# Performance work log

Measured on AMD Instinct MI355X. Metric: run time of the kernel, lower is better.

## Reference

```python
import jax, jax.numpy as jnp
import numpy as np

P, B, L = 32, 64, 128
E, HB, HP = 64, 128, 128   # byte emb dim, byte GRU hidden, packet GRU hidden
PE = 2 * HB                # packet embedding dim = 256
LH = 128                   # attention linear hidden
NC = 10                    # num classes


def _gru_dir(x, w_ih, w_hh, b_ih, b_hh, reverse=False):
    # x: [T, N, E_in] -> outputs [T, N, H]; PyTorch GRU gate math, h0 = 0.
    H = w_hh.shape[1]
    xg = jnp.einsum('tne,ge->tng', x, w_ih) + b_ih  # precompute input gates [T,N,3H]
    if reverse:
        xg = xg[::-1]

    def step(h, xgt):
        hg = h @ w_hh.T + b_hh
        xr, xz, xn = jnp.split(xgt, 3, axis=-1)
        hr, hz, hn = jnp.split(hg, 3, axis=-1)
        r = jax.nn.sigmoid(xr + hr)
        z = jax.nn.sigmoid(xz + hz)
        n = jnp.tanh(xn + r * hn)
        h = (1.0 - z) * n + z * h
        return h, h

    h0 = jnp.zeros((x.shape[1], H), x.dtype)
    _, ys = jax.lax.scan(step, h0, xg)
    if reverse:
        ys = ys[::-1]
    return ys


def _bigru(x, wif, whf, bif, bhf, wib, whb, bib, bhb):
    f = _gru_dir(x, wif, whf, bif, bhf, reverse=False)
    b = _gru_dir(x, wib, whb, bib, bhb, reverse=True)
    return jnp.concatenate([f, b], axis=-1)


def setup_inputs() -> dict:
    key = jax.random.key(0)
    ks = jax.random.split(key, 32)
    rn = lambda k, shp: (jax.random.normal(k, shp, dtype=jnp.float32) * 0.05)
    inp = {}
    inp['flow'] = jax.random.randint(ks[0], (P, B, L), 0, 256, dtype=jnp.int64)
    inp['emb'] = rn(ks[1], (256, E))
    # byte biGRU (forward / backward dirs)
    inp['byte_wih_f'] = rn(ks[2], (3 * HB, E)); inp['byte_whh_f'] = rn(ks[3], (3 * HB, HB))
    inp['byte_bih_f'] = rn(ks[4], (3 * HB,));   inp['byte_bhh_f'] = rn(ks[5], (3 * HB,))
    inp['byte_wih_b'] = rn(ks[6], (3 * HB, E)); inp['byte_whh_b'] = rn(ks[7], (3 * HB, HB))
    inp['byte_bih_b'] = rn(ks[8], (3 * HB,));   inp['byte_bhh_b'] = rn(ks[9], (3 * HB,))
    # packet biGRU
    inp['pkt_wih_f'] = rn(ks[10], (3 * HP, PE)); inp['pkt_whh_f'] = rn(ks[11], (3 * HP, HP))
    inp['pkt_bih_f'] = rn(ks[12], (3 * HP,));    inp['pkt_bhh_f'] = rn(ks[13], (3 * HP,))
    inp['pkt_wih_b'] = rn(ks[14], (3 * HP, PE)); inp['pkt_whh_b'] = rn(ks[15], (3 * HP, HP))
    inp['pkt_bih_b'] = rn(ks[16], (3 * HP,));    inp['pkt_bhh_b'] = rn(ks[17], (3 * HP,))
    # byte attention (Linear(2HB->LH), Linear(LH->1))
    inp['ba_w1'] = rn(ks[18], (LH, 2 * HB)); inp['ba_b1'] = rn(ks[19], (LH,))
    inp['ba_w2'] = rn(ks[20], (1, LH));      inp['ba_b2'] = rn(ks[21], (1,))
    # packet attention (Linear(2HP->LH), Linear(LH->1))
    inp['pa_w1'] = rn(ks[22], (LH, 2 * HP)); inp['pa_b1'] = rn(ks[23], (LH,))
    inp['pa_w2'] = rn(ks[24], (1, LH));      inp['pa_b2'] = rn(ks[25], (1,))
    # final classifier
    inp['wf'] = rn(ks[26], (NC, 2 * HP)); inp['bf'] = rn(ks[27], (NC,))
    return inp


def reference(flow, emb,
              byte_wih_f, byte_whh_f, byte_bih_f, byte_bhh_f,
              byte_wih_b, byte_whh_b, byte_bih_b, byte_bhh_b,
              pkt_wih_f, pkt_whh_f, pkt_bih_f, pkt_bhh_f,
              pkt_wih_b, pkt_whh_b, pkt_bih_b, pkt_bhh_b,
              ba_w1, ba_b1, ba_w2, ba_b2,
              pa_w1, pa_b1, pa_w2, pa_b2,
              wf, bf):
    p, b, l = flow.shape
    x = emb[flow]                                   # [P,B,L,E]
    # batch the per-packet byte GRU across packets: [L, P*B, E]
    xb = x.transpose(2, 0, 1, 3).reshape(l, p * b, E)
    out = _bigru(xb, byte_wih_f, byte_whh_f, byte_bih_f, byte_bhh_f,
                 byte_wih_b, byte_whh_b, byte_bih_b, byte_bhh_b)  # [L, P*B, 2HB]
    out = out.reshape(l, p, b, 2 * HB)
    # Attention: tanh(lin1) -> lin2 -> softmax over dim=1 of the [L,B,1] view,
    # i.e. over the batch axis (faithful to the original code).
    h = jnp.tanh(jnp.einsum('lpbd,hd->lpbh', out, ba_w1) + ba_b1)
    score = jnp.einsum('lpbh,oh->lpbo', h, ba_w2) + ba_b2          # [L,P,B,1]
    attn = jax.nn.softmax(score, axis=2)
    packet_emb = (out * attn).sum(axis=0)                          # [P,B,2HB]
    # packet biGRU over packet sequence
    out2 = _bigru(packet_emb, pkt_wih_f, pkt_whh_f, pkt_bih_f, pkt_bhh_f,
                  pkt_wih_b, pkt_whh_b, pkt_bih_b, pkt_bhh_b)      # [P,B,2HP]
    h2 = jnp.tanh(jnp.einsum('pbd,hd->pbh', out2, pa_w1) + pa_b1)
    score2 = jnp.einsum('pbh,oh->pbo', h2, pa_w2) + pa_b2          # [P,B,1]
    attn2 = jax.nn.softmax(score2, axis=1)
    flow_emb = (out2 * attn2).sum(axis=1)                          # [P,2HP] (faithful sum over dim=1)
    return flow_emb @ wf.T + bf                                    # [P,NC]
```

## Files before the change

kernel.cpp:

```cpp
#include <hip/hip_runtime.h>
#include <hip/hip_bf16.h>
#include <hip/hip_fp16.h>
#include <cstdint>
#include <cstddef>


#define DINLINE __device__ __forceinline__

typedef _Float16 f16;
typedef f16 f16x8 __attribute__((ext_vector_type(8)));
typedef float f32x4 __attribute__((ext_vector_type(4)));

static DINLINE float fast_sigmoid(float x) {
    const float e = __builtin_amdgcn_exp2f(-1.44269504089f * x);
    return __builtin_amdgcn_rcpf(1.0f + e);
}
static DINLINE float fast_tanh(float x) {
    const float e = __builtin_amdgcn_exp2f(2.88539008178f * x);
    return 1.0f - 2.0f * __builtin_amdgcn_rcpf(1.0f + e);
}

static DINLINE void lds_barrier() {
    asm volatile("s_waitcnt lgkmcnt(0)\n\ts_barrier" ::: "memory");
}

__global__ void k_tables(const float* __restrict__ emb,
                         const float* __restrict__ wihF, const float* __restrict__ bihF,
                         const float* __restrict__ bhhF,
                         const float* __restrict__ wihB, const float* __restrict__ bihB,
                         const float* __restrict__ bhhB,
                         __half* __restrict__ tab4F, __half* __restrict__ tab4B) {
    const int v = blockIdx.x & 255;
    const int dir = blockIdx.x >> 8;
    const float* wih = dir ? wihB : wihF;
    const float* bih = dir ? bihB : bihF;
    const float* bhh = dir ? bhhB : bhhF;
    __half* tab4 = dir ? tab4B : tab4F;
    __shared__ float er[64];
    __shared__ float sh[384];
    if (threadIdx.x < 64) er[threadIdx.x] = emb[v * 64 + threadIdx.x];
    __syncthreads();
    const int g = threadIdx.x;
    float acc = bih[g] + (g < 256 ? bhh[g] : 0.0f);
    #pragma unroll
    for (int e = 0; e < 64; ++e) acc = fmaf(wih[g * 64 + e], er[e], acc);
    sh[g] = acc;
    __syncthreads();
    if (g < 128) {
        f16 pk[4];
        pk[0] = (f16)sh[g];
        pk[1] = (f16)sh[g + 128];
        pk[2] = (f16)sh[g + 256];
        pk[3] = (f16)0.f;
        *reinterpret_cast<uint2*>(&tab4[(v * 128 + g) * 4]) =
            *reinterpret_cast<const uint2*>(pk);
    }
}

struct TransArgs {
    const float* src[2];
    float* dst[2];
    int R[2];
    int C[2];
};
__global__ void k_transpose(TransArgs a) {
    const int m = blockIdx.y;
    const float* __restrict__ s = a.src[m];
    float* __restrict__ d = a.dst[m];
    const int R = a.R[m], C = a.C[m];
    const int total = R * C;
    for (int idx = blockIdx.x * blockDim.x + threadIdx.x; idx < total;
         idx += gridDim.x * blockDim.x) {
        const int r = idx / C, c = idx - r * C;
        d[c * R + r] = s[idx];
    }
}

__global__ __launch_bounds__(512, 1) void k_byte_gru(
    const int* __restrict__ flow,
    const __half* __restrict__ tab4F, const __half* __restrict__ tab4B,
    const float* __restrict__ whhF, const float* __restrict__ whhB,
    const float* __restrict__ bhhF, const float* __restrict__ bhhB,
    __half* __restrict__ hF, __half* __restrict__ hB) {
    const int dir = blockIdx.x & 1;
    const int chunk = blockIdx.x >> 1;
    const int row0 = chunk * 16;
    const int tid = threadIdx.x;
    const int wid = tid >> 6;
    const int lane = tid & 63;
    const int c = lane & 15;
    const int q = lane >> 4;
    const int j = wid * 16 + c;

    const uint2* __restrict__ t4 =
        reinterpret_cast<const uint2*>(dir ? tab4B : tab4F);
    const float* __restrict__ whh = dir ? whhB : whhF;
    const float* __restrict__ bhh = dir ? bhhB : bhhF;
    __half* __restrict__ hout = dir ? hB : hF;

    __shared__ f16 hbuf[2][16 * 128];
    __shared__ int flow_lds[16][128];

    for (int i = tid; i < 16 * 128; i += 512)
        flow_lds[i >> 7][i & 127] = flow[row0 * 128 + i] & 255;
    for (int i = tid; i < 16 * 128; i += 512) hbuf[0][i] = (f16)0.f;

    f16x8 Bf[3][4];
    #pragma unroll
    for (int g = 0; g < 3; ++g) {
        #pragma unroll
        for (int ks = 0; ks < 4; ++ks) {
            const float* src = whh + (size_t)(g * 128 + j) * 128 + ks * 32 + q * 8;
            f16x8 b;
            #pragma unroll
            for (int e = 0; e < 8; ++e) b[e] = (f16)src[e];
            Bf[g][ks] = b;
        }
    }
    const float bh2 = bhh[j + 256];
    float hold[4];
    #pragma unroll
    for (int rr = 0; rr < 4; ++rr) hold[rr] = 0.f;
    __syncthreads();

    uint2 xg[4];
    {
        const int tt0 = dir ? 127 : 0;
        #pragma unroll
        for (int rr = 0; rr < 4; ++rr)
            xg[rr] = t4[flow_lds[q * 4 + rr][tt0] * 128 + j];
    }

    #pragma unroll 2
    for (int t = 0; t < 128; ++t) {
        const int curb = t & 1, nxtb = curb ^ 1;
        const int tt = dir ? (127 - t) : t;

        f16x8 Af[4];
        #pragma unroll
        for (int ks = 0; ks < 4; ++ks) {
            const int kb = ks * 32 + q * 8;
            const int idx = c * 128 + (kb ^ ((c & 7) << 3));
            Af[ks] = *reinterpret_cast<const f16x8*>(&hbuf[curb][idx]);
        }

        uint2 xgn[4];
        if (t < 127) {
            const int ttn = dir ? (126 - t) : (t + 1);
            #pragma unroll
            for (int rr = 0; rr < 4; ++rr)
                xgn[rr] = t4[flow_lds[q * 4 + rr][ttn] * 128 + j];
        }

        f32x4 a0 = {0.f, 0.f, 0.f, 0.f};
        f32x4 a1 = {0.f, 0.f, 0.f, 0.f};
        f32x4 a2 = {0.f, 0.f, 0.f, 0.f};
        #pragma unroll
        for (int ks = 0; ks < 4; ++ks) {
            a0 = __builtin_amdgcn_mfma_f32_16x16x32_f16(Af[ks], Bf[0][ks], a0, 0, 0, 0);
            a1 = __builtin_amdgcn_mfma_f32_16x16x32_f16(Af[ks], Bf[1][ks], a1, 0, 0, 0);
            a2 = __builtin_amdgcn_mfma_f32_16x16x32_f16(Af[ks], Bf[2][ks], a2, 0, 0, 0);
        }

        #pragma unroll
        for (int rr = 0; rr < 4; ++rr) {
            const f16* xp = reinterpret_cast<const f16*>(&xg[rr]);
            const float rg = fast_sigmoid((float)xp[0] + a0[rr]);
            const float zg = fast_sigmoid((float)xp[1] + a1[rr]);
            const float ng = fast_tanh((float)xp[2] + rg * (a2[rr] + bh2));
            const float hn = fmaf(zg, hold[rr] - ng, ng);
            hold[rr] = hn;
            const int row = q * 4 + rr;
            hbuf[nxtb][row * 128 + (j ^ ((row & 7) << 3))] = (f16)hn;
            hout[((size_t)tt * 2048 + row0 + row) * 128 + j] = (__half)hn;
        }
        lds_barrier();
        #pragma unroll
        for (int rr = 0; rr < 4; ++rr) xg[rr] = xgn[rr];
    }
}

__global__ __launch_bounds__(256, 1) void k_scores_attn(
    const __half* __restrict__ hF, const __half* __restrict__ hB,
    const float* __restrict__ w1,
    const float* __restrict__ b1, const float* __restrict__ w2,
    const float* __restrict__ b2, float* __restrict__ attn) {
    __shared__ f16 w1lds[128 * 256];
    __shared__ float sc[128];
    const int tid = threadIdx.x;
    for (int i = tid; i < 128 * 256; i += 256) {
        const int col = i >> 8, k = i & 255;
        w1lds[col * 256 + (k ^ ((col & 7) << 3))] = (f16)w1[i];
    }
    const int lane = tid & 63, w = tid >> 6;
    const int c = lane & 15, q = lane >> 4;

    float b1v[8], w2v[8];
    #pragma unroll
    for (int ct = 0; ct < 8; ++ct) {
        b1v[ct] = b1[ct * 16 + c];
        w2v[ct] = w2[ct * 16 + c];
    }
    const float b2v = b2[0];
    __syncthreads();

    for (int it = 0; it < 4; ++it) {
        const int pos0 = blockIdx.x * 512 + it * 128;

        f16x8 Af[2][8];
        #pragma unroll
        for (int pt = 0; pt < 2; ++pt) {
            const size_t pos = (size_t)pos0 + (w * 2 + pt) * 16 + c;
            const f16* hFp = (const f16*)(hF + pos * 128);
            const f16* hBp = (const f16*)(hB + pos * 128);
            #pragma unroll
            for (int ks = 0; ks < 4; ++ks)
                Af[pt][ks] = *reinterpret_cast<const f16x8*>(hFp + ks * 32 + q * 8);
            #pragma unroll
            for (int ks = 0; ks < 4; ++ks)
                Af[pt][4 + ks] = *reinterpret_cast<const f16x8*>(hBp + ks * 32 + q * 8);
        }

        float s[2][4] = {{0.f, 0.f, 0.f, 0.f}, {0.f, 0.f, 0.f, 0.f}};
        #pragma unroll
        for (int ct = 0; ct < 8; ++ct) {
            const int jj = ct * 16 + c;
            f16x8 Bfr[8];
            #pragma unroll
            for (int ks = 0; ks < 8; ++ks) {
                const int k = ks * 32 + q * 8;
                Bfr[ks] = *reinterpret_cast<const f16x8*>(
                    &w1lds[jj * 256 + (k ^ ((jj & 7) << 3))]);
            }
            #pragma unroll
            for (int pt = 0; pt < 2; ++pt) {
                f32x4 acc = {0.f, 0.f, 0.f, 0.f};
                #pragma unroll
                for (int ks = 0; ks < 8; ++ks)
                    acc = __builtin_amdgcn_mfma_f32_16x16x32_f16(Af[pt][ks],
                                                                 Bfr[ks], acc,
                                                                 0, 0, 0);
                #pragma unroll
                for (int rr = 0; rr < 4; ++rr)
                    s[pt][rr] += w2v[ct] * fast_tanh(acc[rr] + b1v[ct]);
            }
        }
        #pragma unroll
        for (int pt = 0; pt < 2; ++pt) {
            #pragma unroll
            for (int rr = 0; rr < 4; ++rr) {
                float v = s[pt][rr];
                v += __shfl_xor(v, 1);
                v += __shfl_xor(v, 2);
                v += __shfl_xor(v, 4);
                v += __shfl_xor(v, 8);
                if (c == 0) sc[(w * 2 + pt) * 16 + q * 4 + rr] = v + b2v;
            }
        }
        __syncthreads();
        if (tid < 128) {
            const float sv = sc[tid];
            float m = sv;
            for (int off = 32; off; off >>= 1) m = fmaxf(m, __shfl_xor(m, off));
            const float e = __expf(sv - m);
            float sum = e;
            for (int off = 32; off; off >>= 1) sum += __shfl_xor(sum, off);
            attn[pos0 + tid] = e / sum;
        }
        __syncthreads();
    }
}

__global__ __launch_bounds__(256) void k_packet_emb(
    const __half* __restrict__ hF, const __half* __restrict__ hB,
    const float* __restrict__ attn, float* __restrict__ pe) {
    const int tid = threadIdx.x;
    const int g = tid >> 6;
    const int lane = tid & 63;
    const int n = blockIdx.x * 4 + g;
    const bool isF = lane < 32;
    const int chunk = lane & 31;
    const __half* __restrict__ hsrc = (isF ? hF : hB) + (size_t)n * 128 + chunk * 4;
    float acc0 = 0.f, acc1 = 0.f, acc2 = 0.f, acc3 = 0.f;
    #pragma unroll 4
    for (int l = 0; l < 128; ++l) {
        const float wv = attn[l * 2048 + n];
        const uint2 u = *reinterpret_cast<const uint2*>(hsrc + (size_t)l * 2048 * 128);
        const f16* hv = reinterpret_cast<const f16*>(&u);
        acc0 = fmaf(wv, (float)hv[0], acc0);
        acc1 = fmaf(wv, (float)hv[1], acc1);
        acc2 = fmaf(wv, (float)hv[2], acc2);
        acc3 = fmaf(wv, (float)hv[3], acc3);
    }
    float4 o = {acc0, acc1, acc2, acc3};
    *reinterpret_cast<float4*>(&pe[n * 256 + (isF ? 0 : 128) + chunk * 4]) = o;
}

__global__ __launch_bounds__(384) void k_pkt_xg(
    const float* __restrict__ pe, const float* __restrict__ wihTF,
    const float* __restrict__ bihF, const float* __restrict__ bhhF,
    const float* __restrict__ wihTB, const float* __restrict__ bihB,
    const float* __restrict__ bhhB, float* __restrict__ xgF,
    float* __restrict__ xgB) {
    const int dir = blockIdx.y;
    const float* __restrict__ wihT = dir ? wihTB : wihTF;
    const float* __restrict__ bih = dir ? bihB : bihF;
    const float* __restrict__ bhh = dir ? bhhB : bhhF;
    float* __restrict__ xg = dir ? xgB : xgF;
    const int rbase = blockIdx.x * 8;
    __shared__ float xrow[8][256];
    for (int i = threadIdx.x; i < 8 * 256; i += 384)
        xrow[i >> 8][i & 255] = pe[rbase * 256 + i];
    __syncthreads();
    const int g = threadIdx.x;
    float acc[8];
    const float bias = bih[g] + (g < 256 ? bhh[g] : 0.0f);
    #pragma unroll
    for (int r = 0; r < 8; ++r) acc[r] = bias;
    for (int d = 0; d < 256; ++d) {
        const float w = wihT[d * 384 + g];
        #pragma unroll
        for (int r = 0; r < 8; ++r) acc[r] = fmaf(w, xrow[r][d], acc[r]);
    }
    #pragma unroll
    for (int r = 0; r < 8; ++r) xg[(rbase + r) * 384 + g] = acc[r];
}

__global__ __launch_bounds__(512, 1) void k_pkt_gru(
    const float* __restrict__ xgF, const float* __restrict__ xgB,
    const float* __restrict__ whhF, const float* __restrict__ whhB,
    const float* __restrict__ bhhF, const float* __restrict__ bhhB,
    float* __restrict__ h2F, float* __restrict__ h2B) {
    const int dir = blockIdx.x & 1;
    const int chunk = blockIdx.x >> 1;
    const int row0 = chunk * 16;
    const int tid = threadIdx.x;
    const int wid = tid >> 6;
    const int lane = tid & 63;
    const int c = lane & 15;
    const int q = lane >> 4;
    const int j = wid * 16 + c;

    const float* __restrict__ xg = dir ? xgB : xgF;
    const float* __restrict__ whh = dir ? whhB : whhF;
    const float* __restrict__ bhh = dir ? bhhB : bhhF;
    float* __restrict__ hout = dir ? h2B : h2F;

    __shared__ f16 hbuf[2][16 * 128];

    for (int i = tid; i < 16 * 128; i += 512) hbuf[0][i] = (f16)0.f;

    f16x8 Bf[3][4];
    #pragma unroll
    for (int g = 0; g < 3; ++g) {
        #pragma unroll
        for (int ks = 0; ks < 4; ++ks) {
            const float* src = whh + (size_t)(g * 128 + j) * 128 + ks * 32 + q * 8;
            f16x8 b;
            #pragma unroll
            for (int e = 0; e < 8; ++e) b[e] = (f16)src[e];
            Bf[g][ks] = b;
        }
    }
    const float bh2 = bhh[j + 256];
    float hold[4];
    #pragma unroll
    for (int rr = 0; rr < 4; ++rr) hold[rr] = 0.f;
    __syncthreads();

    for (int t = 0; t < 32; ++t) {
        const int curb = t & 1, nxtb = curb ^ 1;
        const int tt = dir ? (31 - t) : t;

        float xr[4], xz[4], xn[4];
        #pragma unroll
        for (int rr = 0; rr < 4; ++rr) {
            const float* xp = xg + ((size_t)tt * 64 + row0 + q * 4 + rr) * 384 + j;
            xr[rr] = xp[0];
            xz[rr] = xp[128];
            xn[rr] = xp[256];
        }

        f16x8 Af[4];
        #pragma unroll
        for (int ks = 0; ks < 4; ++ks) {
            const int kb = ks * 32 + q * 8;
            const int idx = c * 128 + (kb ^ ((c & 7) << 3));
            Af[ks] = *reinterpret_cast<const f16x8*>(&hbuf[curb][idx]);
        }

        f32x4 a0 = {0.f, 0.f, 0.f, 0.f};
        f32x4 a1 = {0.f, 0.f, 0.f, 0.f};
        f32x4 a2 = {0.f, 0.f, 0.f, 0.f};
        #pragma unroll
        for (int ks = 0; ks < 4; ++ks) {
            a0 = __builtin_amdgcn_mfma_f32_16x16x32_f16(Af[ks], Bf[0][ks], a0, 0, 0, 0);
            a1 = __builtin_amdgcn_mfma_f32_16x16x32_f16(Af[ks], Bf[1][ks], a1, 0, 0, 0);
            a2 = __builtin_amdgcn_mfma_f32_16x16x32_f16(Af[ks], Bf[2][ks], a2, 0, 0, 0);
        }

        #pragma unroll
        for (int rr = 0; rr < 4; ++rr) {
            const float rg = fast_sigmoid(xr[rr] + a0[rr]);
            const float zg = fast_sigmoid(xz[rr] + a1[rr]);
            const float ng = fast_tanh(xn[rr] + rg * (a2[rr] + bh2));
            const float hn = fmaf(zg, hold[rr] - ng, ng);
            hold[rr] = hn;
            const int row = q * 4 + rr;
            hbuf[nxtb][row * 128 + (j ^ ((row & 7) << 3))] = (f16)hn;
            hout[((size_t)tt * 64 + row0 + row) * 128 + j] = hn;
        }
        lds_barrier();
    }
}

__global__ __launch_bounds__(128) void k_scores2(
    const float* __restrict__ h2F, const float* __restrict__ h2B,
    const float* __restrict__ paw1,
    const float* __restrict__ pab1, const float* __restrict__ paw2,
    const float* __restrict__ pab2, float* __restrict__ scores2) {
    const int n = blockIdx.x;
    const int tid = threadIdx.x;
    __shared__ float x[256];
    __shared__ float red[2];
    x[tid] = h2F[n * 128 + tid];
    x[tid + 128] = h2B[n * 128 + tid];
    __syncthreads();
    float acc = pab1[tid];
    const float* wr = paw1 + tid * 256;
    #pragma unroll 8
    for (int d = 0; d < 256; ++d) acc = fmaf(wr[d], x[d], acc);
    float s = paw2[tid] * fast_tanh(acc);
    s += __shfl_xor(s, 1);
    s += __shfl_xor(s, 2);
    s += __shfl_xor(s, 4);
    s += __shfl_xor(s, 8);
    s += __shfl_xor(s, 16);
    s += __shfl_xor(s, 32);
    if ((tid & 63) == 0) red[tid >> 6] = s;
    __syncthreads();
    if (tid == 0) scores2[n] = red[0] + red[1] + pab2[0];
}

__global__ __launch_bounds__(256) void k_final3(
    const float* __restrict__ h2F, const float* __restrict__ h2B,
    const float* __restrict__ scores2, const float* __restrict__ wf,
    const float* __restrict__ bfv, float* __restrict__ outp) {
    const int p = blockIdx.x;
    const int tid = threadIdx.x;
    __shared__ float sc[64];
    __shared__ float femb[256];
    __shared__ float red[64];

    if (tid < 64) {
        const float s = scores2[p * 64 + tid];
        float m = s;
        for (int off = 32; off; off >>= 1) m = fmaxf(m, __shfl_xor(m, off));
        const float e = __expf(s - m);
        float sum = e;
        for (int off = 32; off; off >>= 1) sum += __shfl_xor(sum, off);
        sc[tid] = e / sum;
    }
    __syncthreads();

    {
        const float* __restrict__ hsrc = (tid < 128) ? h2F : h2B;
        const int d = tid & 127;
        float acc = 0.f;
        for (int b = 0; b < 64; ++b)
            acc = fmaf(sc[b], hsrc[(p * 64 + b) * 128 + d], acc);
        femb[tid] = acc;
    }
    __syncthreads();

    const float fv = femb[tid];
    #pragma unroll
    for (int c = 0; c < 10; ++c) {
        float s = fv * wf[c * 256 + tid];
        s += __shfl_xor(s, 1);
        s += __shfl_xor(s, 2);
        s += __shfl_xor(s, 4);
        s += __shfl_xor(s, 8);
        s += __shfl_xor(s, 16);
        s += __shfl_xor(s, 32);
        if ((tid & 63) == 0) red[(c << 2) | (tid >> 6)] = s;
        __syncthreads();
        if (tid == 0)
            outp[p * 10 + c] = bfv[c] + red[c << 2] + red[(c << 2) | 1] +
                               red[(c << 2) | 2] + red[(c << 2) | 3];
        __syncthreads();
    }
}

extern "C" void kernel_launch(void* const* d_in, const int* in_sizes, int n_in,
                              void* d_out, int out_size, void* d_ws,
                              size_t ws_size, hipStream_t stream) {
    const int* flow = (const int*)d_in[0];
    const float* emb = (const float*)d_in[1];
    const float* byte_wih_f = (const float*)d_in[2];
    const float* byte_whh_f = (const float*)d_in[3];
    const float* byte_bih_f = (const float*)d_in[4];
    const float* byte_bhh_f = (const float*)d_in[5];
    const float* byte_wih_b = (const float*)d_in[6];
    const float* byte_whh_b = (const float*)d_in[7];
    const float* byte_bih_b = (const float*)d_in[8];
    const float* byte_bhh_b = (const float*)d_in[9];
    const float* pkt_wih_f = (const float*)d_in[10];
    const float* pkt_whh_f = (const float*)d_in[11];
    const float* pkt_bih_f = (const float*)d_in[12];
    const float* pkt_bhh_f = (const float*)d_in[13];
    const float* pkt_wih_b = (const float*)d_in[14];
    const float* pkt_whh_b = (const float*)d_in[15];
    const float* pkt_bih_b = (const float*)d_in[16];
    const float* pkt_bhh_b = (const float*)d_in[17];
    const float* ba_w1 = (const float*)d_in[18];
    const float* ba_b1 = (const float*)d_in[19];
    const float* ba_w2 = (const float*)d_in[20];
    const float* ba_b2 = (const float*)d_in[21];
    const float* pa_w1 = (const float*)d_in[22];
    const float* pa_b1 = (const float*)d_in[23];
    const float* pa_w2 = (const float*)d_in[24];
    const float* pa_b2 = (const float*)d_in[25];
    const float* wf = (const float*)d_in[26];
    const float* bf = (const float*)d_in[27];

    char* base = (char*)d_ws;
    size_t off = 0;
    auto allocf = [&](size_t nf) -> float* {
        float* p = (float*)(base + off);
        off += nf * sizeof(float);
        return p;
    };
    auto alloch = [&](size_t nh) -> __half* {
        off = (off + 255) & ~(size_t)255;
        __half* p = (__half*)(base + off);
        off += nh * sizeof(__half);
        return p;
    };
    float* wihTpF = allocf(256 * 384);
    float* wihTpB = allocf(256 * 384);
    float* attn = allocf(262144);
    float* pe = allocf(2048 * 256);
    float* xgF = allocf(32 * 64 * 384);
    float* xgB = allocf(32 * 64 * 384);
    float* h2F = allocf(32 * 64 * 128);
    float* h2B = allocf(32 * 64 * 128);
    float* scores2 = allocf(2048);
    __half* tab4F = alloch(256 * 128 * 4);
    __half* tab4B = alloch(256 * 128 * 4);
    __half* hF = alloch((size_t)128 * 2048 * 128);
    __half* hB = alloch((size_t)128 * 2048 * 128);
    if (off > ws_size) return;
    (void)in_sizes; (void)n_in; (void)out_size;

    k_tables<<<512, 384, 0, stream>>>(emb, byte_wih_f, byte_bih_f, byte_bhh_f,
                                      byte_wih_b, byte_bih_b, byte_bhh_b,
                                      tab4F, tab4B);

    TransArgs ta;
    ta.src[0] = pkt_wih_f; ta.dst[0] = wihTpF; ta.R[0] = 384; ta.C[0] = 256;
    ta.src[1] = pkt_wih_b; ta.dst[1] = wihTpB; ta.R[1] = 384; ta.C[1] = 256;
    k_transpose<<<dim3(96, 2), 256, 0, stream>>>(ta);

    k_byte_gru<<<256, 512, 0, stream>>>(flow, tab4F, tab4B, byte_whh_f,
                                        byte_whh_b, byte_bhh_f, byte_bhh_b, hF,
                                        hB);

    k_scores_attn<<<512, 256, 0, stream>>>(hF, hB, ba_w1, ba_b1, ba_w2, ba_b2,
                                           attn);
    k_packet_emb<<<512, 256, 0, stream>>>(hF, hB, attn, pe);

    k_pkt_xg<<<dim3(256, 2), 384, 0, stream>>>(pe, wihTpF, pkt_bih_f,
                                               pkt_bhh_f, wihTpB, pkt_bih_b,
                                               pkt_bhh_b, xgF, xgB);
    k_pkt_gru<<<8, 512, 0, stream>>>(xgF, xgB, pkt_whh_f, pkt_whh_b,
                                     pkt_bhh_f, pkt_bhh_b, h2F, h2B);
    k_scores2<<<2048, 128, 0, stream>>>(h2F, h2B, pa_w1, pa_b1, pa_w2, pa_b2,
                                        scores2);
    k_final3<<<32, 256, 0, stream>>>(h2F, h2B, scores2, wf, bf, (float*)d_out);
}
```

Baseline: 322.2 us.

## Use fp32 gate tables, packed xg layout, and coalesced h stores in GRUs

The byte GRU gate tables move from packed fp16 to float4 fp32, and the one-step-ahead prefetch of table entries is dropped in favour of loading them at the top of each step. The per-lane fp16 stores of hidden state to global memory are replaced by a cooperative, coalesced 8-byte copy from the LDS h buffer after the barrier. The packet GRU's input-gate precompute now writes an interleaved float4 layout so each step needs one vector load instead of three strided scalar loads. A sched_barrier is added after the LDS barrier, and the removed prefetch may expose table-load latency on the serial recurrence.

```diff
diff --git a/kernel.cpp b/kernel.cpp
--- a/kernel.cpp
+++ b/kernel.cpp
@@ -22,6 +22,7 @@
 
 static DINLINE void lds_barrier() {
     asm volatile("s_waitcnt lgkmcnt(0)\n\ts_barrier" ::: "memory");
+    __builtin_amdgcn_sched_barrier(0);
 }
 
 __global__ void k_tables(const float* __restrict__ emb,
@@ -29,13 +30,13 @@
                          const float* __restrict__ bhhF,
                          const float* __restrict__ wihB, const float* __restrict__ bihB,
                          const float* __restrict__ bhhB,
-                         __half* __restrict__ tab4F, __half* __restrict__ tab4B) {
+                         float4* __restrict__ tab4F, float4* __restrict__ tab4B) {
     const int v = blockIdx.x & 255;
     const int dir = blockIdx.x >> 8;
     const float* wih = dir ? wihB : wihF;
     const float* bih = dir ? bihB : bihF;
     const float* bhh = dir ? bhhB : bhhF;
-    __half* tab4 = dir ? tab4B : tab4F;
+    float4* tab4 = dir ? tab4B : tab4F;
     __shared__ float er[64];
     __shared__ float sh[384];
     if (threadIdx.x < 64) er[threadIdx.x] = emb[v * 64 + threadIdx.x];
@@ -47,13 +48,12 @@
     sh[g] = acc;
     __syncthreads();
     if (g < 128) {
-        f16 pk[4];
-        pk[0] = (f16)sh[g];
-        pk[1] = (f16)sh[g + 128];
-        pk[2] = (f16)sh[g + 256];
-        pk[3] = (f16)0.f;
-        *reinterpret_cast<uint2*>(&tab4[(v * 128 + g) * 4]) =
-            *reinterpret_cast<const uint2*>(pk);
+        float4 pk;
+        pk.x = sh[g];
+        pk.y = sh[g + 128];
+        pk.z = sh[g + 256];
+        pk.w = 0.f;
+        tab4[v * 128 + g] = pk;
     }
 }
 
@@ -78,7 +78,7 @@
 
 __global__ __launch_bounds__(512, 1) void k_byte_gru(
     const int* __restrict__ flow,
-    const __half* __restrict__ tab4F, const __half* __restrict__ tab4B,
+    const float4* __restrict__ tab4F, const float4* __restrict__ tab4B,
     const float* __restrict__ whhF, const float* __restrict__ whhB,
     const float* __restrict__ bhhF, const float* __restrict__ bhhB,
     __half* __restrict__ hF, __half* __restrict__ hB) {
@@ -92,8 +92,7 @@
     const int q = lane >> 4;
     const int j = wid * 16 + c;
 
-    const uint2* __restrict__ t4 =
-        reinterpret_cast<const uint2*>(dir ? tab4B : tab4F);
+    const float4* __restrict__ t4 = dir ? tab4B : tab4F;
     const float* __restrict__ whh = dir ? whhB : whhF;
     const float* __restrict__ bhh = dir ? bhhB : bhhF;
     __half* __restrict__ hout = dir ? hB : hF;
@@ -123,18 +122,14 @@
     for (int rr = 0; rr < 4; ++rr) hold[rr] = 0.f;
     __syncthreads();
 
-    uint2 xg[4];
-    {
-        const int tt0 = dir ? 127 : 0;
-        #pragma unroll
-        for (int rr = 0; rr < 4; ++rr)
-            xg[rr] = t4[flow_lds[q * 4 + rr][tt0] * 128 + j];
-    }
-
-    #pragma unroll 2
     for (int t = 0; t < 128; ++t) {
         const int curb = t & 1, nxtb = curb ^ 1;
         const int tt = dir ? (127 - t) : t;
+
+        float4 x4[4];
+        #pragma unroll
+        for (int rr = 0; rr < 4; ++rr)
+            x4[rr] = t4[flow_lds[q * 4 + rr][tt] * 128 + j];
 
         f16x8 Af[4];
         #pragma unroll
@@ -144,14 +139,6 @@
             Af[ks] = *reinterpret_cast<const f16x8*>(&hbuf[curb][idx]);
         }
 
-        uint2 xgn[4];
-        if (t < 127) {
-            const int ttn = dir ? (126 - t) : (t + 1);
-            #pragma unroll
-            for (int rr = 0; rr < 4; ++rr)
-                xgn[rr] = t4[flow_lds[q * 4 + rr][ttn] * 128 + j];
-        }
-
         f32x4 a0 = {0.f, 0.f, 0.f, 0.f};
         f32x4 a1 = {0.f, 0.f, 0.f, 0.f};
         f32x4 a2 = {0.f, 0.f, 0.f, 0.f};
@@ -164,19 +151,24 @@
 
         #pragma unroll
         for (int rr = 0; rr < 4; ++rr) {
-            const f16* xp = reinterpret_cast<const f16*>(&xg[rr]);
-            const float rg = fast_sigmoid((float)xp[0] + a0[rr]);
-            const float zg = fast_sigmoid((float)xp[1] + a1[rr]);
-            const float ng = fast_tanh((float)xp[2] + rg * (a2[rr] + bh2));
+            const float rg = fast_sigmoid(x4[rr].x + a0[rr]);
+            const float zg = fast_sigmoid(x4[rr].y + a1[rr]);
+            const float ng = fast_tanh(x4[rr].z + rg * (a2[rr] + bh2));
             const float hn = fmaf(zg, hold[rr] - ng, ng);
             hold[rr] = hn;
             const int row = q * 4 + rr;
             hbuf[nxtb][row * 128 + (j ^ ((row & 7) << 3))] = (f16)hn;
-            hout[((size_t)tt * 2048 + row0 + row) * 128 + j] = (__half)hn;
         }
         lds_barrier();
-        #pragma unroll
-        for (int rr = 0; rr < 4; ++rr) xg[rr] = xgn[rr];
+
+        {
+            const int row = tid >> 5;
+            const int ho = (tid & 31) * 4;
+            const int idx = row * 128 + (ho ^ ((row & 7) << 3));
+            const uint2 v = *reinterpret_cast<const uint2*>(&hbuf[nxtb][idx]);
+            *reinterpret_cast<uint2*>(
+                &hout[((size_t)tt * 2048 + row0 + row) * 128 + ho]) = v;
+        }
     }
 }
 
@@ -300,15 +292,16 @@
     const float* __restrict__ pe, const float* __restrict__ wihTF,
     const float* __restrict__ bihF, const float* __restrict__ bhhF,
     const float* __restrict__ wihTB, const float* __restrict__ bihB,
-    const float* __restrict__ bhhB, float* __restrict__ xgF,
-    float* __restrict__ xgB) {
+    const float* __restrict__ bhhB, float4* __restrict__ xg4F,
+    float4* __restrict__ xg4B) {
     const int dir = blockIdx.y;
     const float* __restrict__ wihT = dir ? wihTB : wihTF;
     const float* __restrict__ bih = dir ? bihB : bihF;
     const float* __restrict__ bhh = dir ? bhhB : bhhF;
-    float* __restrict__ xg = dir ? xgB : xgF;
+    float4* __restrict__ xg4 = dir ? xg4B : xg4F;
     const int rbase = blockIdx.x * 8;
     __shared__ float xrow[8][256];
+    __shared__ float sh[8][384];
     for (int i = threadIdx.x; i < 8 * 256; i += 384)
         xrow[i >> 8][i & 255] = pe[rbase * 256 + i];
     __syncthreads();
@@ -323,11 +316,21 @@
         for (int r = 0; r < 8; ++r) acc[r] = fmaf(w, xrow[r][d], acc[r]);
     }
     #pragma unroll
-    for (int r = 0; r < 8; ++r) xg[(rbase + r) * 384 + g] = acc[r];
+    for (int r = 0; r < 8; ++r) sh[r][g] = acc[r];
+    __syncthreads();
+    for (int i = threadIdx.x; i < 8 * 128; i += 384) {
+        const int r = i >> 7, jj = i & 127;
+        float4 pk;
+        pk.x = sh[r][jj];
+        pk.y = sh[r][jj + 128];
+        pk.z = sh[r][jj + 256];
+        pk.w = 0.f;
+        xg4[(size_t)(rbase + r) * 128 + jj] = pk;
+    }
 }
 
 __global__ __launch_bounds__(512, 1) void k_pkt_gru(
-    const float* __restrict__ xgF, const float* __restrict__ xgB,
+    const float4* __restrict__ xg4F, const float4* __restrict__ xg4B,
     const float* __restrict__ whhF, const float* __restrict__ whhB,
     const float* __restrict__ bhhF, const float* __restrict__ bhhB,
     float* __restrict__ h2F, float* __restrict__ h2B) {
@@ -341,7 +344,7 @@
     const int q = lane >> 4;
     const int j = wid * 16 + c;
 
-    const float* __restrict__ xg = dir ? xgB : xgF;
+    const float4* __restrict__ xg4 = dir ? xg4B : xg4F;
     const float* __restrict__ whh = dir ? whhB : whhF;
     const float* __restrict__ bhh = dir ? bhhB : bhhF;
     float* __restrict__ hout = dir ? h2B : h2F;
@@ -372,14 +375,10 @@
         const int curb = t & 1, nxtb = curb ^ 1;
         const int tt = dir ? (31 - t) : t;
 
-        float xr[4], xz[4], xn[4];
-        #pragma unroll
-        for (int rr = 0; rr < 4; ++rr) {
-            const float* xp = xg + ((size_t)tt * 64 + row0 + q * 4 + rr) * 384 + j;
-            xr[rr] = xp[0];
-            xz[rr] = xp[128];
-            xn[rr] = xp[256];
-        }
+        float4 x4[4];
+        #pragma unroll
+        for (int rr = 0; rr < 4; ++rr)
+            x4[rr] = xg4[(size_t)(tt * 64 + row0 + q * 4 + rr) * 128 + j];
 
         f16x8 Af[4];
         #pragma unroll
@@ -401,9 +400,9 @@
 
         #pragma unroll
         for (int rr = 0; rr < 4; ++rr) {
-            const float rg = fast_sigmoid(xr[rr] + a0[rr]);
-            const float zg = fast_sigmoid(xz[rr] + a1[rr]);
-            const float ng = fast_tanh(xn[rr] + rg * (a2[rr] + bh2));
+            const float rg = fast_sigmoid(x4[rr].x + a0[rr]);
+            const float zg = fast_sigmoid(x4[rr].y + a1[rr]);
+            const float ng = fast_tanh(x4[rr].z + rg * (a2[rr] + bh2));
             const float hn = fmaf(zg, hold[rr] - ng, ng);
             hold[rr] = hn;
             const int row = q * 4 + rr;
@@ -541,13 +540,13 @@
     float* wihTpB = allocf(256 * 384);
     float* attn = allocf(262144);
     float* pe = allocf(2048 * 256);
-    float* xgF = allocf(32 * 64 * 384);
-    float* xgB = allocf(32 * 64 * 384);
+    float4* tab4F = (float4*)allocf(256 * 128 * 4);
+    float4* tab4B = (float4*)allocf(256 * 128 * 4);
+    float4* xg4F = (float4*)allocf((size_t)2048 * 128 * 4);
+    float4* xg4B = (float4*)allocf((size_t)2048 * 128 * 4);
     float* h2F = allocf(32 * 64 * 128);
     float* h2B = allocf(32 * 64 * 128);
     float* scores2 = allocf(2048);
-    __half* tab4F = alloch(256 * 128 * 4);
-    __half* tab4B = alloch(256 * 128 * 4);
     __half* hF = alloch((size_t)128 * 2048 * 128);
     __half* hB = alloch((size_t)128 * 2048 * 128);
     if (off > ws_size) return;
@@ -572,8 +571,8 @@
 
     k_pkt_xg<<<dim3(256, 2), 384, 0, stream>>>(pe, wihTpF, pkt_bih_f,
                                                pkt_bhh_f, wihTpB, pkt_bih_b,
-                                               pkt_bhh_b, xgF, xgB);
-    k_pkt_gru<<<8, 512, 0, stream>>>(xgF, xgB, pkt_whh_f, pkt_whh_b,
+                                               pkt_bhh_b, xg4F, xg4B);
+    k_pkt_gru<<<8, 512, 0, stream>>>(xg4F, xg4B, pkt_whh_f, pkt_whh_b,
                                      pkt_bhh_f, pkt_bhh_b, h2F, h2B);
     k_scores2<<<2048, 128, 0, stream>>>(h2F, h2B, pa_w1, pa_b1, pa_w2, pa_b2,
                                         scores2);
```

New measurement: 288.4 us. 10.5% less time.
